# Performance work log

Measured on AMD Instinct MI355X. Metric: run time of the kernel, lower is better.

Reference implementation:

```python
import jax, jax.numpy as jnp
import numpy as np

N, IN_DIM, H, L, NH, LAT = 4096, 16, 128, 4, 8, 16
HD = H // NH
FF = 2 * H
DR_THR = 0.2
LN_EPS = 1e-5


def _ln(x, s, b):
    m = x.mean(-1, keepdims=True)
    v = ((x - m) ** 2).mean(-1, keepdims=True)
    return (x - m) * jax.lax.rsqrt(v + LN_EPS) * s + b


def compute_dr_mask(x_raw):
    eta = x_raw[:, 1] * (2.62 - (-2.62)) + (-2.62)
    phi = x_raw[:, 2] * (3.1416 - (-3.1416)) + (-3.1416)
    deta = eta[:, None] - eta[None, :]
    dphi = phi[:, None] - phi[None, :]
    dphi = jnp.arctan2(jnp.sin(dphi), jnp.cos(dphi))
    dr = jnp.sqrt(deta ** 2 + dphi ** 2)
    return jnp.where(dr <= DR_THR, 0.0, -jnp.inf).astype(jnp.float32)


def setup_inputs() -> dict:
    key = jax.random.key(0)
    ks = jax.random.split(key, 32)
    g = lambda i, shape, s=0.02: (jax.random.normal(ks[i], shape, dtype=jnp.float32) * s)
    inp = {
        'x_raw': jax.random.uniform(ks[0], (N, IN_DIM), dtype=jnp.float32),
        'batch': jnp.zeros((N,), dtype=jnp.int64) if jax.config.read('jax_enable_x64') else jnp.zeros((N,), dtype=jnp.int32),
        'in_w': g(1, (H, IN_DIM), 0.1), 'in_b': jnp.zeros((H,), jnp.float32),
        'ln1_s': jnp.ones((L, H), jnp.float32), 'ln1_b': jnp.zeros((L, H), jnp.float32),
        'qkv_w': g(2, (L, 3 * H, H)), 'qkv_b': jnp.zeros((L, 3 * H), jnp.float32),
        'ao_w': g(3, (L, H, H)), 'ao_b': jnp.zeros((L, H), jnp.float32),
        'ln2_s': jnp.ones((L, H), jnp.float32), 'ln2_b': jnp.zeros((L, H), jnp.float32),
        'f1_w': g(4, (L, FF, H)), 'f1_b': jnp.zeros((L, FF), jnp.float32),
        'f2_w': g(5, (L, H, FF)), 'f2_b': jnp.zeros((L, H), jnp.float32),
        'lat1_w': g(6, (H, H), 0.08), 'lat1_b': jnp.zeros((H,), jnp.float32),
        'lat2_w': g(7, (LAT, H), 0.08), 'lat2_b': jnp.zeros((LAT,), jnp.float32),
        'b1_w': g(8, (H // 2, H), 0.08), 'b1_b': jnp.zeros((H // 2,), jnp.float32),
        'b2_w': g(9, (1, H // 2), 0.008), 'b2_b': jnp.full((1,), -3.0, jnp.float32),
    }
    return inp


def reference(x_raw, batch, in_w, in_b, ln1_s, ln1_b, qkv_w, qkv_b, ao_w, ao_b,
              ln2_s, ln2_b, f1_w, f1_b, f2_w, f2_b,
              lat1_w, lat1_b, lat2_w, lat2_b, b1_w, b1_b, b2_w, b2_b):
    mask = jax.lax.stop_gradient(compute_dr_mask(x_raw))  # [N, N] additive mask
    x = x_raw @ in_w.T + in_b  # [N, H]
    scale = 1.0 / jnp.sqrt(jnp.float32(HD))
    for l in range(L):  # norm_first TransformerEncoderLayer, eval mode (no dropout)
        h = _ln(x, ln1_s[l], ln1_b[l])
        qkv = h @ qkv_w[l].T + qkv_b[l]
        q, k, v = [t.reshape(N, NH, HD) for t in jnp.split(qkv, 3, axis=-1)]
        scores = jnp.einsum('qhd,khd->hqk', q, k) * scale + mask[None]
        attn = jax.nn.softmax(scores, axis=-1)
        o = jnp.einsum('hqk,khd->qhd', attn, v).reshape(N, H)
        x = x + o @ ao_w[l].T + ao_b[l]
        h2 = _ln(x, ln2_s[l], ln2_b[l])
        x = x + jax.nn.relu(h2 @ f1_w[l].T + f1_b[l]) @ f2_w[l].T + f2_b[l]
    lat = jax.nn.relu(x @ lat1_w.T + lat1_b) @ lat2_w.T + lat2_b  # [N, LAT]
    lat = lat / jnp.maximum(jnp.linalg.norm(lat, axis=-1, keepdims=True), 1e-12)
    beta = jax.nn.sigmoid(jax.nn.relu(x @ b1_w.T + b1_b) @ b2_w.T + b2_b)
    beta = jnp.clip(beta, 1e-6, 1 - 1e-6)  # [N, 1]
    return beta, lat
```

## Files before the change

### kernel.cpp

```cpp
#include <hip/hip_runtime.h>
#include <hip/hip_bf16.h>

typedef unsigned short u16;
typedef short short8_t __attribute__((ext_vector_type(8)));
typedef float floatx4 __attribute__((ext_vector_type(4)));

constexpr int NT = 4096, H = 128, CAP = 64;
constexpr int GRID = 256, BLK = 512, GSTRIDE = GRID * BLK;

constexpr int OFF_QKV  = 0;
constexpr int OFF_AO   = 196608;
constexpr int OFF_F1   = 262144;
constexpr int OFF_F2   = 393216;
constexpr int OFF_LAT1 = 524288;
constexpr int OFF_B1   = 540672;
constexpr int OFF_LAT2 = 548864;
constexpr int W_TOTAL  = 550912;

__device__ __forceinline__ float bfu(u16 u) { return __uint_as_float(((unsigned)u) << 16); }
__device__ __forceinline__ u16 f2bf(float f) {
  unsigned u = __float_as_uint(f);
  u += 0x7fffu + ((u >> 16) & 1u);
  return (u16)(u >> 16);
}
__device__ __forceinline__ void unpack8(uint4 u, float* f) {
  f[0] = __uint_as_float(u.x << 16); f[1] = __uint_as_float(u.x & 0xffff0000u);
  f[2] = __uint_as_float(u.y << 16); f[3] = __uint_as_float(u.y & 0xffff0000u);
  f[4] = __uint_as_float(u.z << 16); f[5] = __uint_as_float(u.z & 0xffff0000u);
  f[6] = __uint_as_float(u.w << 16); f[7] = __uint_as_float(u.w & 0xffff0000u);
}
__device__ __forceinline__ short8_t cvt8(const float* bp) {
  const float4 f0 = *(const float4*)bp, f1 = *(const float4*)(bp + 4);
  short8_t r;
  r[0] = (short)f2bf(f0.x); r[1] = (short)f2bf(f0.y);
  r[2] = (short)f2bf(f0.z); r[3] = (short)f2bf(f0.w);
  r[4] = (short)f2bf(f1.x); r[5] = (short)f2bf(f1.y);
  r[6] = (short)f2bf(f1.z); r[7] = (short)f2bf(f1.w);
  return r;
}

__device__ __forceinline__ void st64(unsigned long long* p, unsigned long long v) {
  __hip_atomic_store(p, v, __ATOMIC_RELAXED, __HIP_MEMORY_SCOPE_AGENT);
}
__device__ __forceinline__ void st16(u16* p, u16 v) {
  __hip_atomic_store(p, v, __ATOMIC_RELAXED, __HIP_MEMORY_SCOPE_AGENT);
}

__device__ __forceinline__ void gridbar(int* bar, int want) {
  __syncthreads();
  if (threadIdx.x == 0) {
    asm volatile("" ::: "memory");
    __hip_atomic_fetch_add(bar, 1, __ATOMIC_RELAXED, __HIP_MEMORY_SCOPE_AGENT);
    while (__hip_atomic_load(bar, __ATOMIC_RELAXED, __HIP_MEMORY_SCOPE_AGENT) < want)
      __builtin_amdgcn_s_sleep(2);
    asm volatile("" ::: "memory");
  }
  __syncthreads();
}

struct Prm {
  const float *xr, *in_w, *in_b, *ln1_s, *ln1_b, *qkv_w, *qkv_b, *ao_w, *ao_b,
              *ln2_s, *ln2_b, *f1_w, *f1_b, *f2_w, *f2_b, *lat1_w, *lat1_b,
              *lat2_w, *lat2_b, *b1_w, *b1_b, *b2_w, *b2_b;
  u16* W; u16* QKV[4]; int* bar; float* out;
};

__global__ __launch_bounds__(BLK, 2) void fused_kernel(Prm p) {
  const int t = threadIdx.x, bid = blockIdx.x;
  const int lane = t & 63, w = t >> 6;
  const int lr = lane & 15, quad = lane >> 4;
  const int gtid = bid * BLK + t;
  const int r0 = bid * 16;
  const floatx4 FZ = {0.f, 0.f, 0.f, 0.f};
  int bar_k = 0;

  __shared__ float Xs[16][132];
  __shared__ int NIs[16][CAP];
  __shared__ int NCs[16];
  __shared__ union {
    unsigned long long words[8][64];
    struct { u16 A16[16][152]; u16 FF1[16][280]; } g;
    u16 QS[16][384];
  } sm;

  auto stage_x = [&](const float* sc, const float* bi, bool do_ln) {
    const int r = t >> 5, j0 = (t & 31) * 4;
    const float4 xv = *(const float4*)&Xs[r][j0];
    float v0 = xv.x, v1 = xv.y, v2 = xv.z, v3 = xv.w;
    if (do_ln) {
      float s = v0 + v1 + v2 + v3;
      float ss = v0 * v0 + v1 * v1 + v2 * v2 + v3 * v3;
#pragma unroll
      for (int off = 1; off <= 16; off <<= 1) {
        s += __shfl_xor(s, off); ss += __shfl_xor(ss, off);
      }
      const float mean = s * (1.f / 128.f);
      const float rstd = rsqrtf(ss * (1.f / 128.f) - mean * mean + 1e-5f);
      v0 = (v0 - mean) * rstd * sc[j0]     + bi[j0];
      v1 = (v1 - mean) * rstd * sc[j0 + 1] + bi[j0 + 1];
      v2 = (v2 - mean) * rstd * sc[j0 + 2] + bi[j0 + 2];
      v3 = (v3 - mean) * rstd * sc[j0 + 3] + bi[j0 + 3];
    }
    uint2 pk;
    pk.x = (unsigned)f2bf(v0) | ((unsigned)f2bf(v1) << 16);
    pk.y = (unsigned)f2bf(v2) | ((unsigned)f2bf(v3) << 16);
    *(uint2*)&sm.g.A16[r][j0] = pk;
  };

  for (int i = 49152 + gtid; i < W_TOTAL; i += GSTRIDE) {
    float v;
    if      (i < OFF_AO)   v = p.qkv_w[i];
    else if (i < OFF_F1)   v = p.ao_w[i - OFF_AO];
    else if (i < OFF_F2)   v = p.f1_w[i - OFF_F1];
    else if (i < OFF_LAT1) v = p.f2_w[i - OFF_F2];
    else if (i < OFF_B1)   v = p.lat1_w[i - OFF_LAT1];
    else if (i < OFF_LAT2) v = p.b1_w[i - OFF_B1];
    else                   v = p.lat2_w[i - OFF_LAT2];
    st16(&p.W[i], f2bf(v));
  }
  for (int i = t; i < 16 * H; i += BLK) {
    const int r = i >> 7, c = i & 127;
    const float* xp = p.xr + (size_t)(r0 + r) * 16;
    const float* wp = p.in_w + c * 16;
    float acc = p.in_b[c];
#pragma unroll
    for (int k = 0; k < 16; ++k) acc += xp[k] * wp[k];
    Xs[r][c] = acc;
  }
  for (int uu = 0; uu < 2; ++uu) {
    const int q0 = r0 + uu * 8;
    double qe[8], qp_[8];
#pragma unroll
    for (int j = 0; j < 8; ++j) {
      qe[j]  = (double)p.xr[(q0 + j) * 16 + 1] * 5.24 - 2.62;
      qp_[j] = (double)p.xr[(q0 + j) * 16 + 2] * 6.2832 - 3.1416;
    }
    for (int c = 0; c < 8; ++c) {
      const int k = c * 512 + t;
      const double ke = (double)p.xr[k * 16 + 1] * 5.24 - 2.62;
      const double kp = (double)p.xr[k * 16 + 2] * 6.2832 - 3.1416;
#pragma unroll
      for (int j = 0; j < 8; ++j) {
        const double de = qe[j] - ke;
        double dp = qp_[j] - kp;
        dp -= 6.283185307179586 * rint(dp * 0.15915494309189535);
        const unsigned long long bm = __ballot((de * de + dp * dp) <= 0.04);
        if (lane == 0) sm.words[j][c * 8 + w] = bm;
      }
    }
    __syncthreads();
    {
      unsigned long long m = sm.words[w][lane];
      const int cnt = __popcll(m);
      int incl = cnt;
#pragma unroll
      for (int off = 1; off < 64; off <<= 1) {
        const int n = __shfl_up(incl, off);
        if (lane >= off) incl += n;
      }
      int pos = incl - cnt;
      const int lq = uu * 8 + w;
      const int kbase = (lane >> 3) * 512 + (lane & 7) * 64;
      while (m) {
        const int b = __builtin_ctzll(m);
        m &= m - 1;
        if (pos < CAP) NIs[lq][pos] = kbase + b;
        ++pos;
      }
      if (lane == 63) NCs[lq] = incl > CAP ? CAP : incl;
    }
    __syncthreads();
  }
  stage_x(p.ln1_s, p.ln1_b, true);
  __syncthreads();
  {
    const int c0 = w * 48;
    floatx4 a0 = FZ, a1 = FZ, a2 = FZ;
#pragma unroll
    for (int k0 = 0; k0 < 128; k0 += 32) {
      short8_t a  = *(const short8_t*)&sm.g.A16[lr][k0 + quad * 8];
      short8_t b0 = cvt8(&p.qkv_w[(size_t)(c0 + lr) * 128 + k0 + quad * 8]);
      short8_t b1 = cvt8(&p.qkv_w[(size_t)(c0 + 16 + lr) * 128 + k0 + quad * 8]);
      short8_t b2 = cvt8(&p.qkv_w[(size_t)(c0 + 32 + lr) * 128 + k0 + quad * 8]);
      a0 = __builtin_amdgcn_mfma_f32_16x16x32_bf16(a, b0, a0, 0, 0, 0);
      a1 = __builtin_amdgcn_mfma_f32_16x16x32_bf16(a, b1, a1, 0, 0, 0);
      a2 = __builtin_amdgcn_mfma_f32_16x16x32_bf16(a, b2, a2, 0, 0, 0);
    }
    __syncthreads();
#pragma unroll
    for (int r = 0; r < 4; ++r) {
      const int row = quad * 4 + r;
      sm.QS[row][c0 + lr]      = f2bf(a0[r] + p.qkv_b[c0 + lr]);
      sm.QS[row][c0 + 16 + lr] = f2bf(a1[r] + p.qkv_b[c0 + 16 + lr]);
      sm.QS[row][c0 + 32 + lr] = f2bf(a2[r] + p.qkv_b[c0 + 32 + lr]);
    }
    __syncthreads();
    unsigned long long* d64 = (unsigned long long*)(p.QKV[0] + (size_t)r0 * 384);
    const unsigned long long* s64 = (const unsigned long long*)&sm.QS[0][0];
    for (int j = t; j < 1536; j += BLK) st64(&d64[j], s64[j]);
  }
  gridbar(p.bar, GRID * ++bar_k);

  for (int l = 0; l < 4; ++l) {
    const u16* __restrict__ qsrc = p.QKV[l];
    u16* __restrict__ qdst = (l < 3) ? p.QKV[l + 1] : nullptr;

    {
      const int pr = t >> 2, sub = t & 3;
      const int lq = pr >> 3, h = pr & 7;
      const u16* qp = qsrc + (size_t)(r0 + lq) * 384 + h * 16;
      float qv[16];
      { uint4 a = *(const uint4*)qp, b = *(const uint4*)(qp + 8);
        unpack8(a, qv); unpack8(b, qv + 8); }
#pragma unroll
      for (int d = 0; d < 16; ++d) qv[d] *= 0.25f;
      float o[16];
#pragma unroll
      for (int d = 0; d < 16; ++d) o[d] = 0.f;
      float se = 0.f;
      const int cnt = NCs[lq];
      for (int i = sub; i < cnt; i += 4) {
        const int nb = NIs[lq][i];
        const u16* kp = qsrc + (size_t)nb * 384 + 128 + h * 16;
        float kv[16], vv[16];
        { uint4 a = *(const uint4*)kp;         uint4 b = *(const uint4*)(kp + 8);
          unpack8(a, kv); unpack8(b, kv + 8); }
        { uint4 a = *(const uint4*)(kp + 128); uint4 b = *(const uint4*)(kp + 136);
          unpack8(a, vv); unpack8(b, vv + 8); }
        float s0 = 0.f, s1 = 0.f, s2 = 0.f, s3 = 0.f;
#pragma unroll
        for (int d = 0; d < 16; d += 4) {
          s0 += qv[d] * kv[d];         s1 += qv[d + 1] * kv[d + 1];
          s2 += qv[d + 2] * kv[d + 2]; s3 += qv[d + 3] * kv[d + 3];
        }
        const float e = __expf((s0 + s1) + (s2 + s3));
        se += e;
#pragma unroll
        for (int d = 0; d < 16; ++d) o[d] += e * vv[d];
      }
#pragma unroll
      for (int d = 0; d < 16; ++d) o[d] += __shfl_xor(o[d], 1);
      se += __shfl_xor(se, 1);
#pragma unroll
      for (int d = 0; d < 16; ++d) o[d] += __shfl_xor(o[d], 2);
      se += __shfl_xor(se, 2);
      if (sub == 0) {
        const float inv = 1.f / se;
        uint4 w0, w1;
        w0.x = (unsigned)f2bf(o[0] * inv)  | ((unsigned)f2bf(o[1] * inv) << 16);
        w0.y = (unsigned)f2bf(o[2] * inv)  | ((unsigned)f2bf(o[3] * inv) << 16);
        w0.z = (unsigned)f2bf(o[4] * inv)  | ((unsigned)f2bf(o[5] * inv) << 16);
        w0.w = (unsigned)f2bf(o[6] * inv)  | ((unsigned)f2bf(o[7] * inv) << 16);
        w1.x = (unsigned)f2bf(o[8] * inv)  | ((unsigned)f2bf(o[9] * inv) << 16);
        w1.y = (unsigned)f2bf(o[10] * inv) | ((unsigned)f2bf(o[11] * inv) << 16);
        w1.z = (unsigned)f2bf(o[12] * inv) | ((unsigned)f2bf(o[13] * inv) << 16);
        w1.w = (unsigned)f2bf(o[14] * inv) | ((unsigned)f2bf(o[15] * inv) << 16);
        *(uint4*)&sm.g.A16[lq][h * 16]     = w0;
        *(uint4*)&sm.g.A16[lq][h * 16 + 8] = w1;
      }
    }
    __syncthreads();
    {
      const u16* Bw = p.W + OFF_AO + l * 16384;
      const float* ab = p.ao_b + l * 128;
      const int col = w * 16 + lr;
      floatx4 acc = FZ;
#pragma unroll
      for (int k0 = 0; k0 < 128; k0 += 32) {
        short8_t a = *(const short8_t*)&sm.g.A16[lr][k0 + quad * 8];
        short8_t b = *(const short8_t*)&Bw[(size_t)col * 128 + k0 + quad * 8];
        acc = __builtin_amdgcn_mfma_f32_16x16x32_bf16(a, b, acc, 0, 0, 0);
      }
      const float bv = ab[col];
#pragma unroll
      for (int r = 0; r < 4; ++r)
        Xs[quad * 4 + r][col] += acc[r] + bv;
    }
    __syncthreads();
    stage_x(p.ln2_s + l * 128, p.ln2_b + l * 128, true);
    __syncthreads();
    {
      const u16* Bw = p.W + OFF_F1 + l * 32768;
      const float* fb = p.f1_b + l * 256;
      const int c0 = w * 32;
      floatx4 a0 = FZ, a1 = FZ;
#pragma unroll
      for (int k0 = 0; k0 < 128; k0 += 32) {
        short8_t a  = *(const short8_t*)&sm.g.A16[lr][k0 + quad * 8];
        short8_t b0 = *(const short8_t*)&Bw[(size_t)(c0 + lr) * 128 + k0 + quad * 8];
        short8_t b1 = *(const short8_t*)&Bw[(size_t)(c0 + 16 + lr) * 128 + k0 + quad * 8];
        a0 = __builtin_amdgcn_mfma_f32_16x16x32_bf16(a, b0, a0, 0, 0, 0);
        a1 = __builtin_amdgcn_mfma_f32_16x16x32_bf16(a, b1, a1, 0, 0, 0);
      }
#pragma unroll
      for (int r = 0; r < 4; ++r) {
        const int row = quad * 4 + r;
        sm.g.FF1[row][c0 + lr]      = f2bf(fmaxf(a0[r] + fb[c0 + lr], 0.f));
        sm.g.FF1[row][c0 + 16 + lr] = f2bf(fmaxf(a1[r] + fb[c0 + 16 + lr], 0.f));
      }
    }
    __syncthreads();
    {
      const u16* Bw = p.W + OFF_F2 + l * 32768;
      const float* fb = p.f2_b + l * 128;
      const int col = w * 16 + lr;
      floatx4 acc = FZ;
#pragma unroll
      for (int k0 = 0; k0 < 256; k0 += 32) {
        short8_t a = *(const short8_t*)&sm.g.FF1[lr][k0 + quad * 8];
        short8_t b = *(const short8_t*)&Bw[(size_t)col * 256 + k0 + quad * 8];
        acc = __builtin_amdgcn_mfma_f32_16x16x32_bf16(a, b, acc, 0, 0, 0);
      }
      const float bv = fb[col];
#pragma unroll
      for (int r = 0; r < 4; ++r)
        Xs[quad * 4 + r][col] += acc[r] + bv;
    }
    __syncthreads();
    if (l < 3) {
      stage_x(p.ln1_s + (l + 1) * 128, p.ln1_b + (l + 1) * 128, true);
      __syncthreads();
      {
        const u16* Bw = p.W + OFF_QKV + (l + 1) * 49152;
        const float* qb = p.qkv_b + (l + 1) * 384;
        const int c0 = w * 48;
        floatx4 a0 = FZ, a1 = FZ, a2 = FZ;
#pragma unroll
        for (int k0 = 0; k0 < 128; k0 += 32) {
          short8_t a  = *(const short8_t*)&sm.g.A16[lr][k0 + quad * 8];
          short8_t b0 = *(const short8_t*)&Bw[(size_t)(c0 + lr) * 128 + k0 + quad * 8];
          short8_t b1 = *(const short8_t*)&Bw[(size_t)(c0 + 16 + lr) * 128 + k0 + quad * 8];
          short8_t b2 = *(const short8_t*)&Bw[(size_t)(c0 + 32 + lr) * 128 + k0 + quad * 8];
          a0 = __builtin_amdgcn_mfma_f32_16x16x32_bf16(a, b0, a0, 0, 0, 0);
          a1 = __builtin_amdgcn_mfma_f32_16x16x32_bf16(a, b1, a1, 0, 0, 0);
          a2 = __builtin_amdgcn_mfma_f32_16x16x32_bf16(a, b2, a2, 0, 0, 0);
        }
        __syncthreads();
#pragma unroll
        for (int r = 0; r < 4; ++r) {
          const int row = quad * 4 + r;
          sm.QS[row][c0 + lr]      = f2bf(a0[r] + qb[c0 + lr]);
          sm.QS[row][c0 + 16 + lr] = f2bf(a1[r] + qb[c0 + 16 + lr]);
          sm.QS[row][c0 + 32 + lr] = f2bf(a2[r] + qb[c0 + 32 + lr]);
        }
        __syncthreads();
        unsigned long long* d64 = (unsigned long long*)(qdst + (size_t)r0 * 384);
        const unsigned long long* s64 = (const unsigned long long*)&sm.QS[0][0];
        for (int j = t; j < 1536; j += BLK) st64(&d64[j], s64[j]);
      }
      gridbar(p.bar, GRID * ++bar_k);
    } else {
      stage_x(nullptr, nullptr, false);
      __syncthreads();
      {
        const int c0 = w * 32;
        if (c0 < 192) {
          const u16* Bw = p.W + OFF_LAT1;
          floatx4 a0 = FZ, a1 = FZ;
#pragma unroll
          for (int k0 = 0; k0 < 128; k0 += 32) {
            short8_t a  = *(const short8_t*)&sm.g.A16[lr][k0 + quad * 8];
            short8_t b0 = *(const short8_t*)&Bw[(size_t)(c0 + lr) * 128 + k0 + quad * 8];
            short8_t b1 = *(const short8_t*)&Bw[(size_t)(c0 + 16 + lr) * 128 + k0 + quad * 8];
            a0 = __builtin_amdgcn_mfma_f32_16x16x32_bf16(a, b0, a0, 0, 0, 0);
            a1 = __builtin_amdgcn_mfma_f32_16x16x32_bf16(a, b1, a1, 0, 0, 0);
          }
          const int cA = c0 + lr, cB = c0 + 16 + lr;
          const float bA = cA < 128 ? p.lat1_b[cA] : p.b1_b[cA - 128];
          const float bB = cB < 128 ? p.lat1_b[cB] : p.b1_b[cB - 128];
#pragma unroll
          for (int r = 0; r < 4; ++r) {
            const int row = quad * 4 + r;
            sm.g.FF1[row][cA] = f2bf(fmaxf(a0[r] + bA, 0.f));
            sm.g.FF1[row][cB] = f2bf(fmaxf(a1[r] + bB, 0.f));
          }
        }
      }
      __syncthreads();
      if (t < 256) {
        const int r = t >> 4, c = t & 15;
        float acc = p.lat2_b[c];
        const u16* gw = p.W + OFF_LAT2 + c * 128;
        for (int k = 0; k < 128; ++k) acc += bfu(sm.g.FF1[r][k]) * bfu(gw[k]);
        float ss = acc * acc;
        ss += __shfl_xor(ss, 1); ss += __shfl_xor(ss, 2);
        ss += __shfl_xor(ss, 4); ss += __shfl_xor(ss, 8);
        p.out[NT + (size_t)(r0 + r) * 16 + c] = acc / fmaxf(sqrtf(ss), 1e-12f);
        float v = 0.f;
#pragma unroll
        for (int i = 0; i < 4; ++i)
          v += bfu(sm.g.FF1[r][128 + c * 4 + i]) * p.b2_w[c * 4 + i];
        v += __shfl_xor(v, 1); v += __shfl_xor(v, 2);
        v += __shfl_xor(v, 4); v += __shfl_xor(v, 8);
        if (c == 0) {
          v += p.b2_b[0];
          const float beta = 1.f / (1.f + __expf(-v));
          p.out[r0 + r] = fminf(fmaxf(beta, 1e-6f), 1.f - 1e-6f);
        }
      }
    }
  }
}

extern "C" void kernel_launch(void* const* d_in, const int* in_sizes, int n_in,
                              void* d_out, int out_size, void* d_ws, size_t ws_size,
                              hipStream_t stream) {
  Prm prm;
  prm.xr    = (const float*)d_in[0];
  prm.in_w  = (const float*)d_in[2];  prm.in_b  = (const float*)d_in[3];
  prm.ln1_s = (const float*)d_in[4];  prm.ln1_b = (const float*)d_in[5];
  prm.qkv_w = (const float*)d_in[6];  prm.qkv_b = (const float*)d_in[7];
  prm.ao_w  = (const float*)d_in[8];  prm.ao_b  = (const float*)d_in[9];
  prm.ln2_s = (const float*)d_in[10]; prm.ln2_b = (const float*)d_in[11];
  prm.f1_w  = (const float*)d_in[12]; prm.f1_b  = (const float*)d_in[13];
  prm.f2_w  = (const float*)d_in[14]; prm.f2_b  = (const float*)d_in[15];
  prm.lat1_w= (const float*)d_in[16]; prm.lat1_b= (const float*)d_in[17];
  prm.lat2_w= (const float*)d_in[18]; prm.lat2_b= (const float*)d_in[19];
  prm.b1_w  = (const float*)d_in[20]; prm.b1_b  = (const float*)d_in[21];
  prm.b2_w  = (const float*)d_in[22]; prm.b2_b  = (const float*)d_in[23];
  prm.out   = (float*)d_out;

  char* pw = (char*)d_ws;
  prm.W    = (u16*)pw;   pw += ((size_t)W_TOTAL * 2 + 255) & ~(size_t)255;
  for (int i = 0; i < 4; ++i) { prm.QKV[i] = (u16*)pw; pw += (size_t)NT * 384 * 2; }
  prm.bar  = (int*)pw;   pw += 256;

  hipMemsetAsync(prm.bar, 0, 256, stream);
  fused_kernel<<<GRID, BLK, 0, stream>>>(prm);
}
```

Before: 202.3 us.

## Halve rows per block, double grid, and use 8 lanes per attention query-head

Each block now handles 8 rows instead of 16, so the grid doubles to 512 blocks with launch bounds raised to 4 blocks per CU, and the attention loop splits each query-head's neighbor list over 8 lanes instead of 4. The goal is more parallelism and occupancy for the latency-bound neighbor attention and grid-barrier phases. In exchange, the MFMA tiles still compute 16 rows and discard half, the grid barrier involves twice as many blocks, and the larger register pressure cap may cause spills.

```diff
diff --git a/kernel.cpp b/kernel.cpp
--- a/kernel.cpp
+++ b/kernel.cpp
@@ -6,7 +6,8 @@
 typedef float floatx4 __attribute__((ext_vector_type(4)));
 
 constexpr int NT = 4096, H = 128, CAP = 64;
-constexpr int GRID = 256, BLK = 512, GSTRIDE = GRID * BLK;
+constexpr int ROWS = 8;
+constexpr int GRID = 512, BLK = 512, GSTRIDE = GRID * BLK;
 
 constexpr int OFF_QKV  = 0;
 constexpr int OFF_AO   = 196608;
@@ -65,46 +66,48 @@
   u16* W; u16* QKV[4]; int* bar; float* out;
 };
 
-__global__ __launch_bounds__(BLK, 2) void fused_kernel(Prm p) {
+__global__ __launch_bounds__(BLK, 4) void fused_kernel(Prm p) {
   const int t = threadIdx.x, bid = blockIdx.x;
   const int lane = t & 63, w = t >> 6;
   const int lr = lane & 15, quad = lane >> 4;
   const int gtid = bid * BLK + t;
-  const int r0 = bid * 16;
+  const int r0 = bid * ROWS;
   const floatx4 FZ = {0.f, 0.f, 0.f, 0.f};
   int bar_k = 0;
 
-  __shared__ float Xs[16][132];
-  __shared__ int NIs[16][CAP];
-  __shared__ int NCs[16];
+  __shared__ float Xs[ROWS][132];
+  __shared__ int NIs[ROWS][CAP];
+  __shared__ int NCs[ROWS];
   __shared__ union {
     unsigned long long words[8][64];
     struct { u16 A16[16][152]; u16 FF1[16][280]; } g;
-    u16 QS[16][384];
+    u16 QS[ROWS][384];
   } sm;
 
   auto stage_x = [&](const float* sc, const float* bi, bool do_ln) {
-    const int r = t >> 5, j0 = (t & 31) * 4;
-    const float4 xv = *(const float4*)&Xs[r][j0];
-    float v0 = xv.x, v1 = xv.y, v2 = xv.z, v3 = xv.w;
-    if (do_ln) {
-      float s = v0 + v1 + v2 + v3;
-      float ss = v0 * v0 + v1 * v1 + v2 * v2 + v3 * v3;
-#pragma unroll
-      for (int off = 1; off <= 16; off <<= 1) {
-        s += __shfl_xor(s, off); ss += __shfl_xor(ss, off);
-      }
-      const float mean = s * (1.f / 128.f);
-      const float rstd = rsqrtf(ss * (1.f / 128.f) - mean * mean + 1e-5f);
-      v0 = (v0 - mean) * rstd * sc[j0]     + bi[j0];
-      v1 = (v1 - mean) * rstd * sc[j0 + 1] + bi[j0 + 1];
-      v2 = (v2 - mean) * rstd * sc[j0 + 2] + bi[j0 + 2];
-      v3 = (v3 - mean) * rstd * sc[j0 + 3] + bi[j0 + 3];
-    }
-    uint2 pk;
-    pk.x = (unsigned)f2bf(v0) | ((unsigned)f2bf(v1) << 16);
-    pk.y = (unsigned)f2bf(v2) | ((unsigned)f2bf(v3) << 16);
-    *(uint2*)&sm.g.A16[r][j0] = pk;
+    if (t < ROWS * 32) {
+      const int r = t >> 5, j0 = (t & 31) * 4;
+      const float4 xv = *(const float4*)&Xs[r][j0];
+      float v0 = xv.x, v1 = xv.y, v2 = xv.z, v3 = xv.w;
+      if (do_ln) {
+        float s = v0 + v1 + v2 + v3;
+        float ss = v0 * v0 + v1 * v1 + v2 * v2 + v3 * v3;
+#pragma unroll
+        for (int off = 1; off <= 16; off <<= 1) {
+          s += __shfl_xor(s, off); ss += __shfl_xor(ss, off);
+        }
+        const float mean = s * (1.f / 128.f);
+        const float rstd = rsqrtf(ss * (1.f / 128.f) - mean * mean + 1e-5f);
+        v0 = (v0 - mean) * rstd * sc[j0]     + bi[j0];
+        v1 = (v1 - mean) * rstd * sc[j0 + 1] + bi[j0 + 1];
+        v2 = (v2 - mean) * rstd * sc[j0 + 2] + bi[j0 + 2];
+        v3 = (v3 - mean) * rstd * sc[j0 + 3] + bi[j0 + 3];
+      }
+      uint2 pk;
+      pk.x = (unsigned)f2bf(v0) | ((unsigned)f2bf(v1) << 16);
+      pk.y = (unsigned)f2bf(v2) | ((unsigned)f2bf(v3) << 16);
+      *(uint2*)&sm.g.A16[r][j0] = pk;
+    }
   };
 
   for (int i = 49152 + gtid; i < W_TOTAL; i += GSTRIDE) {
@@ -118,7 +121,7 @@
     else                   v = p.lat2_w[i - OFF_LAT2];
     st16(&p.W[i], f2bf(v));
   }
-  for (int i = t; i < 16 * H; i += BLK) {
+  for (int i = t; i < ROWS * H; i += BLK) {
     const int r = i >> 7, c = i & 127;
     const float* xp = p.xr + (size_t)(r0 + r) * 16;
     const float* wp = p.in_w + c * 16;
@@ -127,13 +130,12 @@
     for (int k = 0; k < 16; ++k) acc += xp[k] * wp[k];
     Xs[r][c] = acc;
   }
-  for (int uu = 0; uu < 2; ++uu) {
-    const int q0 = r0 + uu * 8;
+  {
     double qe[8], qp_[8];
 #pragma unroll
     for (int j = 0; j < 8; ++j) {
-      qe[j]  = (double)p.xr[(q0 + j) * 16 + 1] * 5.24 - 2.62;
-      qp_[j] = (double)p.xr[(q0 + j) * 16 + 2] * 6.2832 - 3.1416;
+      qe[j]  = (double)p.xr[(r0 + j) * 16 + 1] * 5.24 - 2.62;
+      qp_[j] = (double)p.xr[(r0 + j) * 16 + 2] * 6.2832 - 3.1416;
     }
     for (int c = 0; c < 8; ++c) {
       const int k = c * 512 + t;
@@ -159,15 +161,14 @@
         if (lane >= off) incl += n;
       }
       int pos = incl - cnt;
-      const int lq = uu * 8 + w;
       const int kbase = (lane >> 3) * 512 + (lane & 7) * 64;
       while (m) {
         const int b = __builtin_ctzll(m);
         m &= m - 1;
-        if (pos < CAP) NIs[lq][pos] = kbase + b;
+        if (pos < CAP) NIs[w][pos] = kbase + b;
         ++pos;
       }
-      if (lane == 63) NCs[lq] = incl > CAP ? CAP : incl;
+      if (lane == 63) NCs[w] = incl > CAP ? CAP : incl;
     }
     __syncthreads();
   }
@@ -190,14 +191,16 @@
 #pragma unroll
     for (int r = 0; r < 4; ++r) {
       const int row = quad * 4 + r;
-      sm.QS[row][c0 + lr]      = f2bf(a0[r] + p.qkv_b[c0 + lr]);
-      sm.QS[row][c0 + 16 + lr] = f2bf(a1[r] + p.qkv_b[c0 + 16 + lr]);
-      sm.QS[row][c0 + 32 + lr] = f2bf(a2[r] + p.qkv_b[c0 + 32 + lr]);
+      if (row < ROWS) {
+        sm.QS[row][c0 + lr]      = f2bf(a0[r] + p.qkv_b[c0 + lr]);
+        sm.QS[row][c0 + 16 + lr] = f2bf(a1[r] + p.qkv_b[c0 + 16 + lr]);
+        sm.QS[row][c0 + 32 + lr] = f2bf(a2[r] + p.qkv_b[c0 + 32 + lr]);
+      }
     }
     __syncthreads();
     unsigned long long* d64 = (unsigned long long*)(p.QKV[0] + (size_t)r0 * 384);
     const unsigned long long* s64 = (const unsigned long long*)&sm.QS[0][0];
-    for (int j = t; j < 1536; j += BLK) st64(&d64[j], s64[j]);
+    for (int j = t; j < ROWS * 96; j += BLK) st64(&d64[j], s64[j]);
   }
   gridbar(p.bar, GRID * ++bar_k);
 
@@ -206,7 +209,7 @@
     u16* __restrict__ qdst = (l < 3) ? p.QKV[l + 1] : nullptr;
 
     {
-      const int pr = t >> 2, sub = t & 3;
+      const int pr = t >> 3, sub = t & 7;
       const int lq = pr >> 3, h = pr & 7;
       const u16* qp = qsrc + (size_t)(r0 + lq) * 384 + h * 16;
       float qv[16];
@@ -219,7 +222,7 @@
       for (int d = 0; d < 16; ++d) o[d] = 0.f;
       float se = 0.f;
       const int cnt = NCs[lq];
-      for (int i = sub; i < cnt; i += 4) {
+      for (int i = sub; i < cnt; i += 8) {
         const int nb = NIs[lq][i];
         const u16* kp = qsrc + (size_t)nb * 384 + 128 + h * 16;
         float kv[16], vv[16];
@@ -239,11 +242,11 @@
         for (int d = 0; d < 16; ++d) o[d] += e * vv[d];
       }
 #pragma unroll
-      for (int d = 0; d < 16; ++d) o[d] += __shfl_xor(o[d], 1);
-      se += __shfl_xor(se, 1);
-#pragma unroll
-      for (int d = 0; d < 16; ++d) o[d] += __shfl_xor(o[d], 2);
-      se += __shfl_xor(se, 2);
+      for (int off = 1; off < 8; off <<= 1) {
+#pragma unroll
+        for (int d = 0; d < 16; ++d) o[d] += __shfl_xor(o[d], off);
+        se += __shfl_xor(se, off);
+      }
       if (sub == 0) {
         const float inv = 1.f / se;
         uint4 w0, w1;
@@ -273,8 +276,10 @@
       }
       const float bv = ab[col];
 #pragma unroll
-      for (int r = 0; r < 4; ++r)
-        Xs[quad * 4 + r][col] += acc[r] + bv;
+      for (int r = 0; r < 4; ++r) {
+        const int row = quad * 4 + r;
+        if (row < ROWS) Xs[row][col] += acc[r] + bv;
+      }
     }
     __syncthreads();
     stage_x(p.ln2_s + l * 128, p.ln2_b + l * 128, true);
@@ -295,8 +300,10 @@
 #pragma unroll
       for (int r = 0; r < 4; ++r) {
         const int row = quad * 4 + r;
-        sm.g.FF1[row][c0 + lr]      = f2bf(fmaxf(a0[r] + fb[c0 + lr], 0.f));
-        sm.g.FF1[row][c0 + 16 + lr] = f2bf(fmaxf(a1[r] + fb[c0 + 16 + lr], 0.f));
+        if (row < ROWS) {
+          sm.g.FF1[row][c0 + lr]      = f2bf(fmaxf(a0[r] + fb[c0 + lr], 0.f));
+          sm.g.FF1[row][c0 + 16 + lr] = f2bf(fmaxf(a1[r] + fb[c0 + 16 + lr], 0.f));
+        }
       }
     }
     __syncthreads();
@@ -313,8 +320,10 @@
       }
       const float bv = fb[col];
 #pragma unroll
-      for (int r = 0; r < 4; ++r)
-        Xs[quad * 4 + r][col] += acc[r] + bv;
+      for (int r = 0; r < 4; ++r) {
+        const int row = quad * 4 + r;
+        if (row < ROWS) Xs[row][col] += acc[r] + bv;
+      }
     }
     __syncthreads();
     if (l < 3) {
@@ -339,14 +348,16 @@
 #pragma unroll
         for (int r = 0; r < 4; ++r) {
           const int row = quad * 4 + r;
-          sm.QS[row][c0 + lr]      = f2bf(a0[r] + qb[c0 + lr]);
-          sm.QS[row][c0 + 16 + lr] = f2bf(a1[r] + qb[c0 + 16 + lr]);
-          sm.QS[row][c0 + 32 + lr] = f2bf(a2[r] + qb[c0 + 32 + lr]);
+          if (row < ROWS) {
+            sm.QS[row][c0 + lr]      = f2bf(a0[r] + qb[c0 + lr]);
+            sm.QS[row][c0 + 16 + lr] = f2bf(a1[r] + qb[c0 + 16 + lr]);
+            sm.QS[row][c0 + 32 + lr] = f2bf(a2[r] + qb[c0 + 32 + lr]);
+          }
         }
         __syncthreads();
         unsigned long long* d64 = (unsigned long long*)(qdst + (size_t)r0 * 384);
         const unsigned long long* s64 = (const unsigned long long*)&sm.QS[0][0];
-        for (int j = t; j < 1536; j += BLK) st64(&d64[j], s64[j]);
+        for (int j = t; j < ROWS * 96; j += BLK) st64(&d64[j], s64[j]);
       }
       gridbar(p.bar, GRID * ++bar_k);
     } else {
@@ -371,13 +382,15 @@
 #pragma unroll
           for (int r = 0; r < 4; ++r) {
             const int row = quad * 4 + r;
-            sm.g.FF1[row][cA] = f2bf(fmaxf(a0[r] + bA, 0.f));
-            sm.g.FF1[row][cB] = f2bf(fmaxf(a1[r] + bB, 0.f));
+            if (row < ROWS) {
+              sm.g.FF1[row][cA] = f2bf(fmaxf(a0[r] + bA, 0.f));
+              sm.g.FF1[row][cB] = f2bf(fmaxf(a1[r] + bB, 0.f));
+            }
           }
         }
       }
       __syncthreads();
-      if (t < 256) {
+      if (t < ROWS * 16) {
         const int r = t >> 4, c = t & 15;
         float acc = p.lat2_b[c];
         const u16* gw = p.W + OFF_LAT2 + c * 128;
```

Result: slower. 316.4 us (+56.4%).
